# Kernel optimization log

Hardware: AMD Instinct MI355X
Metric: run time of the kernel (lower is better)

The kernel has to match this reference:

```python
import jax, jax.numpy as jnp
import numpy as np

HIDDEN = 4096
N_HEADS = 32
N_KV_HEADS = 8
HEAD_DIM = 128
ROPE_THETA = 1000000.0
EPS = 1e-06
B, T = 1, 2048


def apply_rope(inputs, position_ids, head_dim, theta):
    # inputs: [B, T, H, D], position_ids: [B, T]
    fraction = 2 * jnp.arange(0, head_dim // 2, dtype=jnp.float32) / head_dim
    timescale = jnp.power(theta, fraction)  # [D/2]
    x = (position_ids.astype(jnp.float32)[..., None] / timescale[None, None, :])[..., None, :]  # [B,T,1,D/2]
    sin, cos = jnp.sin(x), jnp.cos(x)
    a, b = jnp.split(inputs, 2, axis=-1)
    return jnp.concatenate([a * cos - b * sin, b * cos + a * sin], axis=-1).astype(inputs.dtype)


def rms_norm(x, weight, eps=EPS):
    rms = jnp.sqrt(jnp.mean(x * x, axis=-1, keepdims=True) + eps)
    return weight * x / rms


def setup_inputs() -> dict:
    key = jax.random.key(0)
    ks = jax.random.split(key, 8)
    lecun = lambda k, shape: jax.random.normal(k, shape, jnp.float32) / np.sqrt(shape[0])
    return {
        "x": jax.random.normal(ks[0], (B, T, HIDDEN), jnp.float32),
        "Wq": lecun(ks[1], (HIDDEN, N_HEADS * HEAD_DIM)),
        "Wk": lecun(ks[2], (HIDDEN, N_KV_HEADS * HEAD_DIM)),
        "Wv": lecun(ks[3], (HIDDEN, N_KV_HEADS * HEAD_DIM)),
        "Wo": lecun(ks[4], (N_HEADS * HEAD_DIM, HIDDEN)),
        "q_norm_w": 1.0 + 0.01 * jax.random.normal(ks[5], (HEAD_DIM,), jnp.float32),
        "k_norm_w": 1.0 + 0.01 * jax.random.normal(ks[6], (HEAD_DIM,), jnp.float32),
        "attention_mask": jnp.ones((B, T), jnp.int32),
        "positions": jnp.broadcast_to(jnp.arange(T, dtype=jnp.int32)[None, :], (B, T)),
    }


def reference(x, Wq, Wk, Wv, Wo, q_norm_w, k_norm_w, attention_mask, positions):
    b, t, _ = x.shape
    q = rms_norm((x @ Wq).reshape(b, t, N_HEADS, HEAD_DIM), q_norm_w)
    k = rms_norm((x @ Wk).reshape(b, t, N_KV_HEADS, HEAD_DIM), k_norm_w)
    v = (x @ Wv).reshape(b, t, N_KV_HEADS, HEAD_DIM)
    q = apply_rope(q, positions, HEAD_DIM, ROPE_THETA)
    k = apply_rope(k, positions, HEAD_DIM, ROPE_THETA)
    # prefill path: kv_cache is None -> causal attention, padding mask on keys
    attn = jax.nn.dot_product_attention(
        q, k, v,
        scale=1.0 / HEAD_DIM ** 0.5,
        mask=attention_mask[:, None, None, :].astype(bool),
        is_causal=True,
    )
    out = attn.reshape(b, t, N_HEADS * HEAD_DIM) @ Wo
    return out, (k, v)
```

## Files before the change

kernel.cpp:

```cpp
#include <hip/hip_runtime.h>


typedef __bf16 bf16;
typedef __bf16 bf16x8 __attribute__((ext_vector_type(8)));
typedef float  f32x4  __attribute__((ext_vector_type(4)));

#define MFMA16(a, b, c) __builtin_amdgcn_mfma_f32_16x16x32_bf16((a), (b), (c), 0, 0, 0)

__device__ __forceinline__ void gll16(const void* g, void* l) {
    __builtin_amdgcn_global_load_lds(
        (const __attribute__((address_space(1))) void*)g,
        (__attribute__((address_space(3))) void*)l,
        16, 0, 0);
}

__global__ __launch_bounds__(256) void detect_convert(
    const unsigned short* __restrict__ probe,
    const void* __restrict__ qw_raw, const void* __restrict__ kw_raw,
    int* __restrict__ flag, bf16* __restrict__ qwc, bf16* __restrict__ kwc) {
    __shared__ int cnt;
    if (threadIdx.x == 0) cnt = 0;
    __syncthreads();
    int local = 0;
    for (int i = 0; i < 4; ++i) {
        const unsigned short w = probe[(threadIdx.x * 4 + i) * 2];
        const int e = (w >> 7) & 0xFF;
        if (e >= 90 && e <= 140) ++local;
    }
    atomicAdd(&cnt, local);
    __syncthreads();
    const bool isbf16 = cnt >= 700;
    if (threadIdx.x == 0) *flag = isbf16 ? 1 : 0;
    const int t = threadIdx.x;
    if (t < 128)
        qwc[t] = isbf16 ? ((const bf16*)qw_raw)[t] : (bf16)((const float*)qw_raw)[t];
    else
        kwc[t - 128] = isbf16 ? ((const bf16*)kw_raw)[t - 128] : (bf16)((const float*)kw_raw)[t - 128];
}

__global__ __launch_bounds__(256) void convert_x(const void* __restrict__ xv,
                                                 bf16* __restrict__ xb,
                                                 const int* __restrict__ flag) {
    const size_t i8 = ((size_t)blockIdx.x * 256 + threadIdx.x) * 8;
    if (*flag) {
        *(bf16x8*)&xb[i8] = *(const bf16x8*)&((const bf16*)xv)[i8];
    } else {
        const f32x4 a = *(const f32x4*)&((const float*)xv)[i8];
        const f32x4 b = *(const f32x4*)&((const float*)xv)[i8 + 4];
        bf16x8 o;
#pragma unroll
        for (int e = 0; e < 4; ++e) { o[e] = (bf16)a[e]; o[e + 4] = (bf16)b[e]; }
        *(bf16x8*)&xb[i8] = o;
    }
}

#define GBM 128
#define GBN 128
#define GBK 64
#define GLD 72

__global__ __launch_bounds__(256) void gemm_nt(
    const bf16* __restrict__ A,
    const void* __restrict__ B1v, const void* __restrict__ B2v, const void* __restrict__ B3v,
    bf16* __restrict__ Cb1, float* __restrict__ Cf1,
    bf16* __restrict__ Cb2, float* __restrict__ Cf2,
    bf16* __restrict__ Cb3, float* __restrict__ Cf3,
    const int* __restrict__ flag, int K,
    int ldb1, int ldb2, int ldb3, int ldc1, int ldc2, int ldc3,
    int ns1, int ns2) {
    __shared__ __align__(16) bf16 As[2][GBM * 64];
    __shared__ __align__(16) bf16 Bs[GBN * GLD];

    const int nbxp = (int)gridDim.x >> 3;
    int id = blockIdx.y * gridDim.x + blockIdx.x;
    const int xcd = id & 7;
    const int j = id >> 3;
    const int bx = xcd * nbxp + j / (int)gridDim.y;
    const int by = j % (int)gridDim.y;

    const void* Bv;
    bf16* Cb;
    float* Cf;
    int n0, ldb, ldc;
    if (bx < ns1) {
        Bv = B1v; Cb = Cb1; Cf = Cf1; n0 = bx * GBN; ldb = ldb1; ldc = ldc1;
    } else if (bx < ns1 + ns2) {
        Bv = B2v; Cb = Cb2; Cf = Cf2; n0 = (bx - ns1) * GBN; ldb = ldb2; ldc = ldc2;
    } else {
        Bv = B3v; Cb = Cb3; Cf = Cf3; n0 = (bx - ns1 - ns2) * GBN; ldb = ldb3; ldc = ldc3;
    }
    const int m0 = by * GBM;

    const bool bBf16 = (*flag) != 0;
    const bf16*  Bb = (const bf16*)Bv;
    const float* Bf = (const float*)Bv;

    const int tid  = threadIdx.x;
    const int wave = tid >> 6;
    const int lane = tid & 63;
    const int l15  = lane & 15;
    const int quad = lane >> 4;
    const int axor = l15 & 7;
    const int wm = (wave >> 1) * 64;
    const int wn = (wave & 1) * 64;

    const int l8 = lane >> 3;
    const bf16* aP = A + (size_t)(m0 + wave * 8 + l8) * K + (((lane & 7) ^ l8) << 3);

    f32x4 acc[4][4];
#pragma unroll
    for (int i = 0; i < 4; ++i)
#pragma unroll
        for (int j2 = 0; j2 < 4; ++j2) acc[i][j2] = {0.f, 0.f, 0.f, 0.f};

    bf16 bReg[4][8];

#define LOAD_B(k0)                                                             \
    {                                                                          \
        if (bBf16) {                                                           \
            _Pragma("unroll")                                                  \
            for (int p = 0; p < 4; ++p) {                                      \
                const int w16 = wave * 4 + p;                                  \
                const int n = (w16 & 1) * 64 + lane, kc = w16 >> 1;            \
                _Pragma("unroll")                                              \
                for (int e = 0; e < 8; ++e)                                    \
                    bReg[p][e] = Bb[(size_t)((k0) + kc * 8 + e) * ldb + n0 + n]; \
            }                                                                  \
        } else {                                                               \
            _Pragma("unroll")                                                  \
            for (int p = 0; p < 4; ++p) {                                      \
                const int w16 = wave * 4 + p;                                  \
                const int n = (w16 & 1) * 64 + lane, kc = w16 >> 1;            \
                _Pragma("unroll")                                              \
                for (int e = 0; e < 8; ++e)                                    \
                    bReg[p][e] = (bf16)Bf[(size_t)((k0) + kc * 8 + e) * ldb + n0 + n]; \
            }                                                                  \
        }                                                                      \
    }

#define GLL_A(k0, buf)                                                         \
    {                                                                          \
        _Pragma("unroll")                                                      \
        for (int p = 0; p < 4; ++p)                                            \
            gll16(aP + (size_t)p * 32 * K + (k0),                              \
                  &As[buf][p * 2048 + wave * 512]);                            \
    }

#define WRITE_B()                                                              \
    {                                                                          \
        _Pragma("unroll")                                                      \
        for (int p = 0; p < 4; ++p) {                                          \
            const int w16 = wave * 4 + p;                                      \
            const int n = (w16 & 1) * 64 + lane, kc = w16 >> 1;                \
            bf16x8 bv;                                                         \
            _Pragma("unroll")                                                  \
            for (int e = 0; e < 8; ++e) bv[e] = bReg[p][e];                    \
            *(bf16x8*)&Bs[n * GLD + kc * 8] = bv;                              \
        }                                                                      \
    }

#define COMPUTE(buf)                                                           \
    {                                                                          \
        _Pragma("unroll")                                                      \
        for (int kk = 0; kk < GBK; kk += 32) {                                 \
            bf16x8 af[4], bfr[4];                                              \
            _Pragma("unroll")                                                  \
            for (int i = 0; i < 4; ++i)                                        \
                af[i] = *(const bf16x8*)&As[buf][(wm + i * 16 + l15) * 64 +    \
                        ((((kk) >> 3) + quad) ^ axor) * 8];                    \
            _Pragma("unroll")                                                  \
            for (int j3 = 0; j3 < 4; ++j3)                                     \
                bfr[j3] = *(const bf16x8*)&Bs[(wn + j3 * 16 + l15) * GLD + kk + quad * 8]; \
            _Pragma("unroll")                                                  \
            for (int i = 0; i < 4; ++i)                                        \
                _Pragma("unroll")                                              \
                for (int j3 = 0; j3 < 4; ++j3)                                 \
                    acc[i][j3] = MFMA16(af[i], bfr[j3], acc[i][j3]);           \
        }                                                                      \
    }

    const int nt = K >> 6;
    LOAD_B(0);
    GLL_A(0, 0);
    WRITE_B();
    __syncthreads();
    int cur = 0;
    for (int t = 0; t < nt; ++t) {
        if (t + 1 < nt) {
            LOAD_B((t + 1) << 6);
            GLL_A((t + 1) << 6, cur ^ 1);
        }
        COMPUTE(cur);
        __syncthreads();
        if (t + 1 < nt) {
            WRITE_B();
            __syncthreads();
        }
        cur ^= 1;
    }
#undef LOAD_B
#undef GLL_A
#undef WRITE_B
#undef COMPUTE

#pragma unroll
    for (int i = 0; i < 4; ++i)
#pragma unroll
        for (int j2 = 0; j2 < 4; ++j2)
#pragma unroll
            for (int r = 0; r < 4; ++r) {
                const int row = m0 + wm + i * 16 + quad * 4 + r;
                const int col = n0 + wn + j2 * 16 + l15;
                const float v = acc[i][j2][r];
                if (Cb) Cb[(size_t)row * ldc + col] = (bf16)v;
                if (Cf) Cf[(size_t)row * ldc + col] = v;
            }
}

__global__ __launch_bounds__(256) void norm_rope(const bf16* __restrict__ src,
                                                 bf16* __restrict__ dst_bf,
                                                 float* __restrict__ dst_f32,
                                                 const bf16* __restrict__ w,
                                                 const int* __restrict__ positions,
                                                 int H) {
    const int wid  = blockIdx.x * 4 + (threadIdx.x >> 6);
    const int lane = threadIdx.x & 63;
    const int token = wid / H, head = wid % H;
    const bf16* s = src + ((size_t)token * H + head) * 128;
    const float f0 = (float)s[lane], f1 = (float)s[lane + 64];
    float ss = f0 * f0 + f1 * f1;
    for (int off = 32; off >= 1; off >>= 1) ss += __shfl_xor(ss, off);
    const float inv_rms = rsqrtf(ss * (1.0f / 128.0f) + 1e-6f);
    const float n0 = f0 * inv_rms * (float)w[lane];
    const float n1 = f1 * inv_rms * (float)w[lane + 64];
    const float pos = (float)positions[token];
    const float inv_ts = __expf((float)lane * (-13.815510557964274f / 64.0f));
    const float ang = pos * inv_ts;
    float sn, cs;
    __sincosf(ang, &sn, &cs);
    const float o0 = n0 * cs - n1 * sn;
    const float o1 = n1 * cs + n0 * sn;
    const size_t base = ((size_t)token * H + head) * 128;
    if (dst_bf)  { dst_bf[base + lane] = (bf16)o0;  dst_bf[base + lane + 64] = (bf16)o1; }
    if (dst_f32) { dst_f32[base + lane] = o0;       dst_f32[base + lane + 64] = o1; }
}

__global__ __launch_bounds__(256) void flash_attn(const bf16* __restrict__ Q,
                                                  const bf16* __restrict__ Kg,
                                                  const bf16* __restrict__ Vg,
                                                  bf16* __restrict__ Og) {
    __shared__ __align__(16) bf16 Ks[32 * 128];
    __shared__ __align__(16) bf16 Vt[128 * 40];
    __shared__ __align__(16) bf16 Ps[4][16 * 40];

    int id = blockIdx.y * 32 + blockIdx.x;
    id = (id & 7) * 128 + (id >> 3);
    const int h  = id >> 5;
    const int qt = 31 - (id & 31);
    const int kvh  = h >> 2;
    const int tid  = threadIdx.x;
    const int wave = tid >> 6;
    const int lane = tid & 63;
    const int l15  = lane & 15;
    const int quad = lane >> 4;
    const int q0   = qt * 64;
    const int qw0  = q0 + wave * 16;
    const int myq  = qw0 + l15;
    const float scale = 0.08838834764831845f;

    bf16x8 qf[4];
    {
        const bf16* qrow = Q + ((size_t)myq * 32 + h) * 128;
#pragma unroll
        for (int kc = 0; kc < 4; ++kc)
            qf[kc] = *(const bf16x8*)&qrow[kc * 32 + quad * 8];
    }

    f32x4 oacc[8];
#pragma unroll
    for (int i = 0; i < 8; ++i) oacc[i] = {0.f, 0.f, 0.f, 0.f};
    float m_run = -1e30f, l_run = 0.f;

    const int ksr  = tid & 31;
    const int kscb = tid >> 5;
    const int vr0  = (tid & 15) * 2;
    const int vcb  = tid >> 4;

    char* kbytes = (char*)Ks;
    char* vbytes = (char*)Vt;
    char* pbytes = (char*)&Ps[wave][0];

    const int ntiles = (q0 + 64) >> 5;
    for (int kt = 0; kt < ntiles; ++kt) {
        const int kb = kt * 32;
        {
            const bf16* src = Kg + ((size_t)(kb + ksr) * 8 + kvh) * 128;
            const bf16x8 v0 = *(const bf16x8*)&src[kscb * 8];
            const bf16x8 v1 = *(const bf16x8*)&src[(kscb + 8) * 8];
            const int b0 = (ksr * 256 + kscb * 16) ^ ((ksr & 7) << 4);
            const int b1 = (ksr * 256 + (kscb + 8) * 16) ^ ((ksr & 7) << 4);
            *(bf16x8*)(kbytes + b0) = v0;
            *(bf16x8*)(kbytes + b1) = v1;
        }
        {
            const bf16* s0 = Vg + ((size_t)(kb + vr0) * 8 + kvh) * 128 + vcb * 8;
            const bf16x8 a = *(const bf16x8*)s0;
            const bf16x8 b = *(const bf16x8*)(s0 + 1024);
#pragma unroll
            for (int e = 0; e < 8; ++e) {
                union { bf16 hh[2]; unsigned int u; } pk;
                pk.hh[0] = a[e]; pk.hh[1] = b[e];
                *(unsigned int*)(vbytes + (vcb * 8 + e) * 80 + vr0 * 2) = pk.u;
            }
        }
        __syncthreads();

        f32x4 sacc[2];
        sacc[0] = {0.f, 0.f, 0.f, 0.f};
        sacc[1] = {0.f, 0.f, 0.f, 0.f};
#pragma unroll
        for (int st = 0; st < 2; ++st) {
            const int row = st * 16 + l15;
#pragma unroll
            for (int kc = 0; kc < 4; ++kc) {
                const int bofs = (row * 256 + kc * 64 + quad * 16) ^ ((row & 7) << 4);
                const bf16x8 kf = *(const bf16x8*)(kbytes + bofs);
                sacc[st] = MFMA16(kf, qf[kc], sacc[st]);
            }
        }

        float sv[8];
        float pm = -1e30f;
#pragma unroll
        for (int st = 0; st < 2; ++st)
#pragma unroll
            for (int r = 0; r < 4; ++r) {
                const int key = kb + st * 16 + quad * 4 + r;
                float s = sacc[st][r] * scale;
                if (key > myq) s = -1e30f;
                sv[st * 4 + r] = s;
                pm = fmaxf(pm, s);
            }
        pm = fmaxf(pm, __shfl_xor(pm, 16));
        pm = fmaxf(pm, __shfl_xor(pm, 32));
        const float m_new = fmaxf(m_run, pm);
        const float corr = __expf(m_run - m_new);
        float ps = 0.f;
        bf16 pb[8];
#pragma unroll
        for (int i = 0; i < 8; ++i) {
            const float p = __expf(sv[i] - m_new);
            ps += p;
            pb[i] = (bf16)p;
        }
        ps += __shfl_xor(ps, 16);
        ps += __shfl_xor(ps, 32);
        l_run = l_run * corr + ps;
        m_run = m_new;

#pragma unroll
        for (int st = 0; st < 2; ++st)
#pragma unroll
            for (int r = 0; r < 4; ++r)
                *(bf16*)(pbytes + l15 * 80 + (st * 16 + quad * 4 + r) * 2) = pb[st * 4 + r];

        float corrq[4];
#pragma unroll
        for (int r = 0; r < 4; ++r) corrq[r] = __shfl(corr, quad * 4 + r);
#pragma unroll
        for (int nt = 0; nt < 8; ++nt)
#pragma unroll
            for (int r = 0; r < 4; ++r) oacc[nt][r] *= corrq[r];

        const bf16x8 pf = *(const bf16x8*)(pbytes + l15 * 80 + quad * 16);
#pragma unroll
        for (int nt = 0; nt < 8; ++nt) {
            const bf16x8 vf = *(const bf16x8*)(vbytes + (nt * 16 + l15) * 80 + quad * 16);
            oacc[nt] = MFMA16(pf, vf, oacc[nt]);
        }
        __syncthreads();
    }

    const float rinv = 1.0f / l_run;
    float linv[4];
#pragma unroll
    for (int r = 0; r < 4; ++r) linv[r] = __shfl(rinv, quad * 4 + r);
#pragma unroll
    for (int nt = 0; nt < 8; ++nt)
#pragma unroll
        for (int r = 0; r < 4; ++r) {
            const int row = qw0 + quad * 4 + r;
            Og[((size_t)row * 32 + h) * 128 + nt * 16 + l15] = (bf16)(oacc[nt][r] * linv[r]);
        }
}

extern "C" void kernel_launch(void* const* d_in, const int* in_sizes, int n_in,
                              void* d_out, int out_size, void* d_ws, size_t ws_size,
                              hipStream_t stream) {
    const void* x  = d_in[0];
    const void* Wq = d_in[1];
    const void* Wk = d_in[2];
    const void* Wv = d_in[3];
    const void* Wo = d_in[4];
    const void* qw = d_in[5];
    const void* kw = d_in[6];
    const int* positions = (const int*)d_in[8];

    char* ws = (char*)d_ws;
    int*  flag    = (int*)ws;
    bf16* qwc     = (bf16*)(ws + 64);
    bf16* kwc     = (bf16*)(ws + 64 + 256);
    bf16* kq      = (bf16*)(ws + 4096);
    bf16* vb      = (bf16*)(ws + 4096 + 4194304);
    bf16* xb      = (bf16*)(ws + 4096 + 8388608);
    bf16* attnbuf = (bf16*)(ws + 4096 + 8388608);

    float* outf = (float*)d_out;
    float* Kof  = outf + 8388608;
    float* Vof  = outf + 10485760;
    bf16*  qb   = (bf16*)d_out;

    detect_convert<<<1, 256, 0, stream>>>((const unsigned short*)Wq, qw, kw, flag, qwc, kwc);
    convert_x<<<4096, 256, 0, stream>>>(x, xb, flag);

    gemm_nt<<<dim3(48, 16), 256, 0, stream>>>(
        xb, Wq, Wk, Wv,
        qb, nullptr, kq, nullptr, vb, Vof,
        flag, 4096,
        4096, 1024, 1024, 4096, 1024, 1024,
        32, 8);

    norm_rope<<<16384, 256, 0, stream>>>(qb, qb, nullptr, qwc, positions, 32);
    norm_rope<<<4096, 256, 0, stream>>>(kq, kq, Kof, kwc, positions, 8);

    flash_attn<<<dim3(32, 32), 256, 0, stream>>>(qb, kq, vb, attnbuf);

    gemm_nt<<<dim3(32, 16), 256, 0, stream>>>(
        attnbuf, Wo, Wo, Wo,
        nullptr, outf, nullptr, nullptr, nullptr, nullptr,
        flag, 4096,
        4096, 4096, 4096, 4096, 4096, 4096,
        32, 0);
}
```

Measured before the change: 639.9 us.

## Pre-transpose QKV weights to bf16 and use a simpler NT-layout GEMM

```diff
diff --git a/kernel.cpp b/kernel.cpp
--- a/kernel.cpp
+++ b/kernel.cpp
@@ -52,6 +52,123 @@
         for (int e = 0; e < 4; ++e) { o[e] = (bf16)a[e]; o[e + 4] = (bf16)b[e]; }
         *(bf16x8*)&xb[i8] = o;
     }
+}
+
+__global__ __launch_bounds__(256) void transpose_w(
+    const void* __restrict__ Wq, const void* __restrict__ Wk, const void* __restrict__ Wv,
+    bf16* __restrict__ WqT, bf16* __restrict__ WkT, bf16* __restrict__ WvT,
+    const int* __restrict__ flag) {
+    __shared__ float T[64][65];
+    int id = blockIdx.x;
+    const void* src;
+    bf16* dst;
+    int N, tn, tk;
+    if (id < 4096) {
+        src = Wq; dst = WqT; N = 4096; tn = id & 63; tk = id >> 6;
+    } else {
+        id -= 4096;
+        if (id < 1024) { src = Wk; dst = WkT; }
+        else           { src = Wv; dst = WvT; id -= 1024; }
+        N = 1024; tn = id & 15; tk = id >> 4;
+    }
+    const int k0 = tk * 64, n0 = tn * 64;
+    const bool bB = (*flag) != 0;
+    const int tx = threadIdx.x & 63, ty = threadIdx.x >> 6;
+#pragma unroll
+    for (int p = 0; p < 16; ++p) {
+        const int k = ty + p * 4;
+        T[k][tx] = bB ? (float)((const bf16*)src)[(size_t)(k0 + k) * N + n0 + tx]
+                      : ((const float*)src)[(size_t)(k0 + k) * N + n0 + tx];
+    }
+    __syncthreads();
+#pragma unroll
+    for (int p = 0; p < 16; ++p) {
+        const int n = ty + p * 4;
+        dst[(size_t)(n0 + n) * 4096 + k0 + tx] = (bf16)T[tx][n];
+    }
+}
+
+__global__ __launch_bounds__(256) void gemm_bt(
+    const bf16* __restrict__ A,
+    const bf16* __restrict__ B1T, const bf16* __restrict__ B2T,
+    bf16* __restrict__ C1, bf16* __restrict__ C2,
+    int K, int ldc1, int ldc2, int ns1) {
+    __shared__ __align__(16) bf16 As[128 * 64];
+    __shared__ __align__(16) bf16 Bs[128 * 64];
+
+    const int nbxp = (int)gridDim.x >> 3;
+    int id = blockIdx.y * gridDim.x + blockIdx.x;
+    const int xcd = id & 7;
+    const int j = id >> 3;
+    const int bx = xcd * nbxp + j / (int)gridDim.y;
+    const int by = j % (int)gridDim.y;
+
+    const bf16* BT;
+    bf16* C;
+    int n0, ldc;
+    if (bx < ns1) { BT = B1T; C = C1; n0 = bx * 128; ldc = ldc1; }
+    else          { BT = B2T; C = C2; n0 = (bx - ns1) * 128; ldc = ldc2; }
+    const int m0 = by * 128;
+
+    const int tid  = threadIdx.x;
+    const int wave = tid >> 6;
+    const int lane = tid & 63;
+    const int l15  = lane & 15;
+    const int quad = lane >> 4;
+    const int axor = l15 & 7;
+    const int wm = (wave >> 1) * 64;
+    const int wn = (wave & 1) * 64;
+    const int l8 = lane >> 3;
+
+    const bf16* aP = A  + (size_t)(m0 + wave * 8 + l8) * K + (((lane & 7) ^ l8) << 3);
+    const bf16* bP = BT + (size_t)(n0 + wave * 8 + l8) * K + (((lane & 7) ^ l8) << 3);
+
+    f32x4 acc[4][4];
+#pragma unroll
+    for (int i = 0; i < 4; ++i)
+#pragma unroll
+        for (int j2 = 0; j2 < 4; ++j2) acc[i][j2] = {0.f, 0.f, 0.f, 0.f};
+
+    const int nt = K >> 6;
+    for (int t = 0; t < nt; ++t) {
+        const int k0 = t << 6;
+#pragma unroll
+        for (int p = 0; p < 4; ++p)
+            gll16(aP + (size_t)p * 32 * K + k0, &As[p * 2048 + wave * 512]);
+#pragma unroll
+        for (int p = 0; p < 4; ++p)
+            gll16(bP + (size_t)p * 32 * K + k0, &Bs[p * 2048 + wave * 512]);
+        __syncthreads();
+#pragma unroll
+        for (int kk = 0; kk < 64; kk += 32) {
+            bf16x8 af[4], bfr[4];
+#pragma unroll
+            for (int i = 0; i < 4; ++i)
+                af[i] = *(const bf16x8*)&As[(wm + i * 16 + l15) * 64 +
+                        (((kk >> 3) + quad) ^ axor) * 8];
+#pragma unroll
+            for (int j3 = 0; j3 < 4; ++j3)
+                bfr[j3] = *(const bf16x8*)&Bs[(wn + j3 * 16 + l15) * 64 +
+                          (((kk >> 3) + quad) ^ axor) * 8];
+#pragma unroll
+            for (int i = 0; i < 4; ++i)
+#pragma unroll
+                for (int j3 = 0; j3 < 4; ++j3)
+                    acc[i][j3] = MFMA16(af[i], bfr[j3], acc[i][j3]);
+        }
+        __syncthreads();
+    }
+
+#pragma unroll
+    for (int i = 0; i < 4; ++i)
+#pragma unroll
+        for (int j2 = 0; j2 < 4; ++j2)
+#pragma unroll
+            for (int r = 0; r < 4; ++r) {
+                const int row = m0 + wm + i * 16 + quad * 4 + r;
+                const int col = n0 + wn + j2 * 16 + l15;
+                C[(size_t)row * ldc + col] = (bf16)acc[i][j2][r];
+            }
 }
 
 #define GBM 128
@@ -245,6 +362,17 @@
     if (dst_f32) { dst_f32[base + lane] = o0;       dst_f32[base + lane + 64] = o1; }
 }
 
+__global__ __launch_bounds__(256) void conv_b2f(const bf16* __restrict__ s,
+                                                float* __restrict__ d) {
+    const size_t i8 = ((size_t)blockIdx.x * 256 + threadIdx.x) * 8;
+    const bf16x8 v = *(const bf16x8*)&s[i8];
+    f32x4 a, b;
+#pragma unroll
+    for (int e = 0; e < 4; ++e) { a[e] = (float)v[e]; b[e] = (float)v[e + 4]; }
+    *(f32x4*)&d[i8] = a;
+    *(f32x4*)&d[i8 + 4] = b;
+}
+
 __global__ __launch_bounds__(256) void flash_attn(const bf16* __restrict__ Q,
                                                   const bf16* __restrict__ Kg,
                                                   const bf16* __restrict__ Vg,
@@ -418,22 +546,25 @@
     float* outf = (float*)d_out;
     float* Kof  = outf + 8388608;
     float* Vof  = outf + 10485760;
-    bf16*  qb   = (bf16*)d_out;
+    bf16*  WqT  = (bf16*)d_out;
+    bf16*  WkT  = (bf16*)((char*)d_out + 33554432);
+    bf16*  WvT  = (bf16*)((char*)d_out + 41943040);
+    bf16*  qb   = (bf16*)((char*)d_out + 33554432);
 
     detect_convert<<<1, 256, 0, stream>>>((const unsigned short*)Wq, qw, kw, flag, qwc, kwc);
     convert_x<<<4096, 256, 0, stream>>>(x, xb, flag);
-
-    gemm_nt<<<dim3(48, 16), 256, 0, stream>>>(
-        xb, Wq, Wk, Wv,
-        qb, nullptr, kq, nullptr, vb, Vof,
-        flag, 4096,
-        4096, 1024, 1024, 4096, 1024, 1024,
-        32, 8);
+    transpose_w<<<6144, 256, 0, stream>>>(Wq, Wk, Wv, WqT, WkT, WvT, flag);
+
+    gemm_bt<<<dim3(16, 16), 256, 0, stream>>>(xb, WkT, WvT, kq, vb, 4096, 1024, 1024, 8);
+    gemm_bt<<<dim3(32, 16), 256, 0, stream>>>(xb, WqT, WqT, qb, qb, 4096, 4096, 4096, 32);
 
     norm_rope<<<16384, 256, 0, stream>>>(qb, qb, nullptr, qwc, positions, 32);
-    norm_rope<<<4096, 256, 0, stream>>>(kq, kq, Kof, kwc, positions, 8);
+    norm_rope<<<4096, 256, 0, stream>>>(kq, kq, nullptr, kwc, positions, 8);
 
     flash_attn<<<dim3(32, 32), 256, 0, stream>>>(qb, kq, vb, attnbuf);
+
+    conv_b2f<<<1024, 256, 0, stream>>>(kq, Kof);
+    conv_b2f<<<1024, 256, 0, stream>>>(vb, Vof);
 
     gemm_nt<<<dim3(32, 16), 256, 0, stream>>>(
         attnbuf, Wo, Wo, Wo,
```

After: 674.4 us. 1.05x slower.
